# Kernel tuning notes

Measured on AMD Instinct MI355X. Metric: run time of the kernel, lower is better.

Reference implementation:

```python
import jax, jax.numpy as jnp
import numpy as np

DEGREE = 8


def setup_inputs() -> dict:
    key = jax.random.key(0)
    k1, k2 = jax.random.split(key)
    x = jax.random.normal(k1, (8192, 1024), dtype=jnp.float32)
    # xavier_normal-ish scale for coeffs [input_dim, output_dim, degree+1]
    std = (2.0 / (1024 + 1024)) ** 0.5
    cheby_coeffs = jax.random.normal(k2, (1024, 1024, DEGREE + 1), dtype=jnp.float32) * std
    return {"x": x, "cheby_coeffs": cheby_coeffs}


def _cheby(x, degree):
    # x: [B, I] in [-1, 1]; returns T: [B, I, degree+1]
    T = [jnp.ones_like(x), x]
    for n in range(2, degree + 1):
        T.append(2.0 * x * T[-1] - T[-2])
    return jnp.stack(T, axis=-1)


def reference(x, cheby_coeffs) -> jnp.ndarray:
    input_dim = cheby_coeffs.shape[0]
    degree = cheby_coeffs.shape[-1] - 1
    x = x.reshape(-1, input_dim)
    xmin = jnp.min(x, axis=1, keepdims=True)
    xmax = jnp.max(x, axis=1, keepdims=True)
    x = 2.0 * (x - xmin) / (xmax - xmin) - 1.0
    T = _cheby(x, degree)  # [B, I, D+1]
    y = jnp.einsum('bij,ioj->bo', T, cheby_coeffs)
    return y
```

## Files before the change

kernel.cpp:

```cpp
#include <hip/hip_runtime.h>
#include <hip/hip_bf16.h>


typedef __attribute__((ext_vector_type(8))) short bf16x8s;
typedef __attribute__((ext_vector_type(4))) float f32x4;

constexpr int BROWS = 8192;
constexpr int IDIM  = 1024;
constexpr int ODIM  = 1024;
constexpr int DEG1  = 9;
constexpr int KP    = 8;
constexpr int KD    = IDIM * KP;

__device__ __forceinline__ ushort f2bf(float f) {
  return ((__hip_bfloat16_raw)__float2bfloat16(f)).x;
}

__device__ __forceinline__ void gload_lds16(const void* g, void* l) {
  __builtin_amdgcn_global_load_lds(
      (const __attribute__((address_space(1))) unsigned int*)g,
      (__attribute__((address_space(3))) unsigned int*)l, 16, 0, 0);
}

__global__ __launch_bounds__(256) void zero_bias_kernel(float* __restrict__ bias) {
  bias[blockIdx.x * 256 + threadIdx.x] = 0.0f;
}

__global__ __launch_bounds__(256) void build_a_kernel(const float* __restrict__ x,
                                                      ushort* __restrict__ A2) {
  __shared__ float red[8];
  const int b = blockIdx.x, t = threadIdx.x, lane = t & 63, wv = t >> 6;
  const float* xr = x + (size_t)b * IDIM;
  const float4 v = ((const float4*)xr)[t];
  float mn = fminf(fminf(v.x, v.y), fminf(v.z, v.w));
  float mx = fmaxf(fmaxf(v.x, v.y), fmaxf(v.z, v.w));
#pragma unroll
  for (int off = 32; off >= 1; off >>= 1) {
    mn = fminf(mn, __shfl_xor(mn, off));
    mx = fmaxf(mx, __shfl_xor(mx, off));
  }
  if (lane == 0) { red[wv] = mn; red[4 + wv] = mx; }
  __syncthreads();
  mn = fminf(fminf(red[0], red[1]), fminf(red[2], red[3]));
  mx = fmaxf(fmaxf(red[4], red[5]), fmaxf(red[6], red[7]));
  const float sc = 2.0f / (mx - mn);
  const float of = -mn * sc - 1.0f;

  uint4* adst = (uint4*)(A2 + (size_t)b * KD);
#pragma unroll
  for (int c = 0; c < 4; ++c) {
    const int i = c * 256 + t;
    const float xn = fmaf(sc, xr[i], of);
    const float T2 = 2.f * xn * xn - 1.f;
    const float T3 = 2.f * xn * T2 - xn;
    const float T4 = 2.f * xn * T3 - T2;
    const float T5 = 2.f * xn * T4 - T3;
    const float T6 = 2.f * xn * T5 - T4;
    const float T7 = 2.f * xn * T6 - T5;
    const float T8 = 2.f * xn * T7 - T6;
    uint4 w;
    w.x = (uint)f2bf(xn) | ((uint)f2bf(T2) << 16);
    w.y = (uint)f2bf(T3) | ((uint)f2bf(T4) << 16);
    w.z = (uint)f2bf(T5) | ((uint)f2bf(T6) << 16);
    w.w = (uint)f2bf(T7) | ((uint)f2bf(T8) << 16);
    adst[i] = w;
  }
}

__global__ __launch_bounds__(256) void build_b_kernel(const float* __restrict__ coeffs,
                                                      ushort* __restrict__ B2T,
                                                      float* __restrict__ bias) {
  __shared__ __align__(16) ushort tile[64 * 256];
  __shared__ float lb[64];
  const int i0 = blockIdx.x * 32;
  const int o0 = blockIdx.y * 64;
  const int t  = threadIdx.x;
  if (t < 64) lb[t] = 0.0f;
  __syncthreads();
  for (int idx = t; idx < 18432; idx += 256) {
    const int i_l = idx / 576;
    const int rem = idx - i_l * 576;
    const float v = coeffs[((size_t)(i0 + i_l) * ODIM + o0) * DEG1 + rem];
    const int o_l = rem / 9;
    const int j   = rem - o_l * 9;
    if (j == 0) atomicAdd(&lb[o_l], v);
    else tile[o_l * 256 + i_l * KP + (j - 1)] = f2bf(v);
  }
  __syncthreads();
  for (int idx = t; idx < 2048; idx += 256) {
    const int o_l = idx >> 5;
    const int w   = idx & 31;
    uint4* gdst = (uint4*)(B2T + (size_t)(o0 + o_l) * KD + i0 * KP);
    gdst[w] = ((const uint4*)tile)[idx];
  }
  if (t < 64) atomicAdd(&bias[o0 + t], lb[t]);
}

__global__ __launch_bounds__(512, 1) void gemm_kernel(const ushort* __restrict__ A2,
                                                      const ushort* __restrict__ B2T,
                                                      const float* __restrict__ bias,
                                                      float* __restrict__ out) {
  constexpr int BK    = 64;
  constexpr int KT    = KD / BK;
  constexpr int ABUF  = 256 * BK;
  constexpr int BBUF  = 128 * BK;
  constexpr int BUFSZ = ABUF + BBUF;
  __shared__ __align__(16) ushort Sm[3 * BUFSZ];

  const int t    = threadIdx.x;
  const int lane = t & 63;
  const int wave = t >> 6;
  const int wr   = wave >> 1;
  const int wc   = wave & 1;
  const int c16  = lane & 15;
  const int quad = lane >> 4;

  const int orig = blockIdx.y * 8 + blockIdx.x;
  const int swz  = (orig & 7) * 32 + (orig >> 3);
  const int rowBase = (swz >> 3) * 256;
  const int colBase = (swz & 7) * 128;

  const int trow = t >> 3;
  const int scol = (t & 7) ^ (trow & 7);
  const ushort* aB = A2  + (size_t)(rowBase + trow) * KD + scol * 8;
  const ushort* bB = B2T + (size_t)(colBase + trow) * KD + scol * 8;
  ushort* uA = Sm + t * 8;
  ushort* uB = Sm + ABUF + t * 8;

  auto issA = [&](int buf, size_t ko, int a) {
    gload_lds16(aB + (size_t)a * (64 * KD) + ko, uA + buf * BUFSZ + a * 4096);
  };
  auto issB = [&](int buf, size_t ko, int b2) {
    gload_lds16(bB + (size_t)b2 * (64 * KD) + ko, uB + buf * BUFSZ + b2 * 4096);
  };

  const int aoff = (wr * 64 + c16) * BK;
  const int boff = (wc * 64 + c16) * BK;
  const int cx0  = ((0 + quad) ^ (c16 & 7)) * 8;
  const int cx1  = ((4 + quad) ^ (c16 & 7)) * 8;

  f32x4 acc[4][4];
#pragma unroll
  for (int m = 0; m < 4; ++m)
#pragma unroll
    for (int n = 0; n < 4; ++n) acc[m][n] = (f32x4){0.f, 0.f, 0.f, 0.f};

  issA(0, 0, 0); issA(0, 0, 1); issA(0, 0, 2); issA(0, 0, 3);
  issB(0, 0, 0); issB(0, 0, 1);
  issA(1, BK, 0); issA(1, BK, 1); issA(1, BK, 2); issA(1, BK, 3);
  issB(1, BK, 0); issB(1, BK, 1);
  asm volatile("s_waitcnt vmcnt(6)" ::: "memory");
  __builtin_amdgcn_s_barrier();

  int cur = 0;
  for (int it = 0; it < KT; ++it) {
    const ushort* Asb = Sm + cur * BUFSZ;
    const ushort* Bsb = Asb + ABUF;
    const int nb = (cur >= 1) ? cur - 1 : 2;
    const size_t ko = (size_t)(it + 2) * BK;
    const bool pf = (it < KT - 2);

    {
      bf16x8s afr[4], bfr[4];
#pragma unroll
      for (int m = 0; m < 4; ++m)
        afr[m] = *(const bf16x8s*)&Asb[aoff + m * (16 * 64) + cx0];
#pragma unroll
      for (int n = 0; n < 4; ++n)
        bfr[n] = *(const bf16x8s*)&Bsb[boff + n * (16 * 64) + cx0];
      if (pf) { issA(nb, ko, 0); issA(nb, ko, 1); issA(nb, ko, 2); }
      __builtin_amdgcn_s_setprio(1);
#pragma unroll
      for (int m = 0; m < 4; ++m)
#pragma unroll
        for (int n = 0; n < 4; ++n)
          acc[m][n] = __builtin_amdgcn_mfma_f32_16x16x32_bf16(afr[m], bfr[n],
                                                              acc[m][n], 0, 0, 0);
      __builtin_amdgcn_s_setprio(0);
    }
    {
      bf16x8s afr[4], bfr[4];
#pragma unroll
      for (int m = 0; m < 4; ++m)
        afr[m] = *(const bf16x8s*)&Asb[aoff + m * (16 * 64) + cx1];
#pragma unroll
      for (int n = 0; n < 4; ++n)
        bfr[n] = *(const bf16x8s*)&Bsb[boff + n * (16 * 64) + cx1];
      if (pf) { issA(nb, ko, 3); issB(nb, ko, 0); issB(nb, ko, 1); }
      __builtin_amdgcn_s_setprio(1);
#pragma unroll
      for (int m = 0; m < 4; ++m)
#pragma unroll
        for (int n = 0; n < 4; ++n)
          acc[m][n] = __builtin_amdgcn_mfma_f32_16x16x32_bf16(afr[m], bfr[n],
                                                              acc[m][n], 0, 0, 0);
      __builtin_amdgcn_s_setprio(0);
    }

    if (pf)              { asm volatile("s_waitcnt vmcnt(6)" ::: "memory"); }
    else if (it == KT-2) { asm volatile("s_waitcnt vmcnt(0)" ::: "memory"); }
    __builtin_amdgcn_s_barrier();

    cur = (cur == 2) ? 0 : cur + 1;
  }

#pragma unroll
  for (int n = 0; n < 4; ++n) {
    const int col = colBase + wc * 64 + n * 16 + c16;
    const float bv = bias[col];
#pragma unroll
    for (int m = 0; m < 4; ++m) {
      const int r0 = rowBase + wr * 64 + m * 16 + quad * 4;
#pragma unroll
      for (int r = 0; r < 4; ++r)
        out[(size_t)(r0 + r) * ODIM + col] = acc[m][n][r] + bv;
    }
  }
}

extern "C" void kernel_launch(void* const* d_in, const int* in_sizes, int n_in,
                              void* d_out, int out_size, void* d_ws, size_t ws_size,
                              hipStream_t stream) {
  const float* x      = (const float*)d_in[0];
  const float* coeffs = (const float*)d_in[1];
  float* out = (float*)d_out;

  char* ws = (char*)d_ws;
  float*  bias = (float*)ws;
  ushort* B2T  = (ushort*)(ws + 65536);
  ushort* A2   = (ushort*)(ws + 65536 + (size_t)ODIM * KD * 2);

  zero_bias_kernel<<<ODIM / 256, 256, 0, stream>>>(bias);
  build_a_kernel<<<BROWS, 256, 0, stream>>>(x, A2);
  build_b_kernel<<<dim3(IDIM / 32, ODIM / 64), 256, 0, stream>>>(coeffs, B2T, bias);
  gemm_kernel<<<dim3(ODIM / 128, BROWS / 256), 512, 0, stream>>>(A2, B2T, bias, out);
}
```

Baseline: 275.8 us.

## Fuse Chebyshev feature expansion into GEMM A-tile loading, drop materialized A

The separate pass that expanded x into a bf16 Chebyshev feature matrix in global memory is removed. A small kernel now computes only per-row min/max scale and offset. The GEMM loads raw x values, evaluates the Chebyshev recurrence in registers and writes bf16 A tiles straight into shared memory, while B keeps its async global-to-LDS prefetch. This avoids writing and re-reading a roughly 128 MB intermediate. In exchange, each column block recomputes the polynomials, and the x-load latency plus the VALU work now sit inside the MFMA pipeline loop.

```diff
diff --git a/kernel.cpp b/kernel.cpp
--- a/kernel.cpp
+++ b/kernel.cpp
@@ -26,12 +26,11 @@
   bias[blockIdx.x * 256 + threadIdx.x] = 0.0f;
 }
 
-__global__ __launch_bounds__(256) void build_a_kernel(const float* __restrict__ x,
-                                                      ushort* __restrict__ A2) {
+__global__ __launch_bounds__(256) void rowstats_kernel(const float* __restrict__ x,
+                                                       float2* __restrict__ stats) {
   __shared__ float red[8];
   const int b = blockIdx.x, t = threadIdx.x, lane = t & 63, wv = t >> 6;
-  const float* xr = x + (size_t)b * IDIM;
-  const float4 v = ((const float4*)xr)[t];
+  const float4 v = ((const float4*)(x + (size_t)b * IDIM))[t];
   float mn = fminf(fminf(v.x, v.y), fminf(v.z, v.w));
   float mx = fmaxf(fmaxf(v.x, v.y), fmaxf(v.z, v.w));
 #pragma unroll
@@ -41,29 +40,11 @@
   }
   if (lane == 0) { red[wv] = mn; red[4 + wv] = mx; }
   __syncthreads();
-  mn = fminf(fminf(red[0], red[1]), fminf(red[2], red[3]));
-  mx = fmaxf(fmaxf(red[4], red[5]), fmaxf(red[6], red[7]));
-  const float sc = 2.0f / (mx - mn);
-  const float of = -mn * sc - 1.0f;
-
-  uint4* adst = (uint4*)(A2 + (size_t)b * KD);
-#pragma unroll
-  for (int c = 0; c < 4; ++c) {
-    const int i = c * 256 + t;
-    const float xn = fmaf(sc, xr[i], of);
-    const float T2 = 2.f * xn * xn - 1.f;
-    const float T3 = 2.f * xn * T2 - xn;
-    const float T4 = 2.f * xn * T3 - T2;
-    const float T5 = 2.f * xn * T4 - T3;
-    const float T6 = 2.f * xn * T5 - T4;
-    const float T7 = 2.f * xn * T6 - T5;
-    const float T8 = 2.f * xn * T7 - T6;
-    uint4 w;
-    w.x = (uint)f2bf(xn) | ((uint)f2bf(T2) << 16);
-    w.y = (uint)f2bf(T3) | ((uint)f2bf(T4) << 16);
-    w.z = (uint)f2bf(T5) | ((uint)f2bf(T6) << 16);
-    w.w = (uint)f2bf(T7) | ((uint)f2bf(T8) << 16);
-    adst[i] = w;
+  if (t == 0) {
+    mn = fminf(fminf(red[0], red[1]), fminf(red[2], red[3]));
+    mx = fmaxf(fmaxf(red[4], red[5]), fmaxf(red[6], red[7]));
+    const float sc = 2.0f / (mx - mn);
+    stats[b] = (float2){sc, -mn * sc - 1.0f};
   }
 }
 
@@ -96,7 +77,8 @@
   if (t < 64) atomicAdd(&bias[o0 + t], lb[t]);
 }
 
-__global__ __launch_bounds__(512, 1) void gemm_kernel(const ushort* __restrict__ A2,
+__global__ __launch_bounds__(512, 1) void gemm_kernel(const float* __restrict__ x,
+                                                      const float2* __restrict__ stats,
                                                       const ushort* __restrict__ B2T,
                                                       const float* __restrict__ bias,
                                                       float* __restrict__ out) {
@@ -122,13 +104,39 @@
 
   const int trow = t >> 3;
   const int scol = (t & 7) ^ (trow & 7);
-  const ushort* aB = A2  + (size_t)(rowBase + trow) * KD + scol * 8;
+  const float*  xB = x + (size_t)(rowBase + trow) * IDIM + scol;
   const ushort* bB = B2T + (size_t)(colBase + trow) * KD + scol * 8;
-  ushort* uA = Sm + t * 8;
   ushort* uB = Sm + ABUF + t * 8;
 
-  auto issA = [&](int buf, size_t ko, int a) {
-    gload_lds16(aB + (size_t)a * (64 * KD) + ko, uA + buf * BUFSZ + a * 4096);
+  float scr[4], ofr[4];
+#pragma unroll
+  for (int a = 0; a < 4; ++a) {
+    const float2 s = stats[rowBase + trow + 64 * a];
+    scr[a] = s.x; ofr[a] = s.y;
+  }
+
+  auto loadX = [&](int it2, float xv[4]) {
+#pragma unroll
+    for (int a = 0; a < 4; ++a) xv[a] = xB[(size_t)a * (64 * IDIM) + it2 * 8];
+  };
+  auto computeA = [&](int buf, const float xv[4]) {
+#pragma unroll
+    for (int a = 0; a < 4; ++a) {
+      const float xn = fmaf(scr[a], xv[a], ofr[a]);
+      const float T2 = 2.f * xn * xn - 1.f;
+      const float T3 = 2.f * xn * T2 - xn;
+      const float T4 = 2.f * xn * T3 - T2;
+      const float T5 = 2.f * xn * T4 - T3;
+      const float T6 = 2.f * xn * T5 - T4;
+      const float T7 = 2.f * xn * T6 - T5;
+      const float T8 = 2.f * xn * T7 - T6;
+      uint4 w;
+      w.x = (uint)f2bf(xn) | ((uint)f2bf(T2) << 16);
+      w.y = (uint)f2bf(T3) | ((uint)f2bf(T4) << 16);
+      w.z = (uint)f2bf(T5) | ((uint)f2bf(T6) << 16);
+      w.w = (uint)f2bf(T7) | ((uint)f2bf(T8) << 16);
+      *(uint4*)&Sm[buf * BUFSZ + a * 4096 + t * 8] = w;
+    }
   };
   auto issB = [&](int buf, size_t ko, int b2) {
     gload_lds16(bB + (size_t)b2 * (64 * KD) + ko, uB + buf * BUFSZ + b2 * 4096);
@@ -145,11 +153,14 @@
 #pragma unroll
     for (int n = 0; n < 4; ++n) acc[m][n] = (f32x4){0.f, 0.f, 0.f, 0.f};
 
-  issA(0, 0, 0); issA(0, 0, 1); issA(0, 0, 2); issA(0, 0, 3);
+  {
+    float xv[4];
+    loadX(0, xv); computeA(0, xv);
+    loadX(1, xv); computeA(1, xv);
+  }
   issB(0, 0, 0); issB(0, 0, 1);
-  issA(1, BK, 0); issA(1, BK, 1); issA(1, BK, 2); issA(1, BK, 3);
   issB(1, BK, 0); issB(1, BK, 1);
-  asm volatile("s_waitcnt vmcnt(6)" ::: "memory");
+  asm volatile("s_waitcnt vmcnt(2) lgkmcnt(0)" ::: "memory");
   __builtin_amdgcn_s_barrier();
 
   int cur = 0;
@@ -160,6 +171,9 @@
     const size_t ko = (size_t)(it + 2) * BK;
     const bool pf = (it < KT - 2);
 
+    float xv[4];
+    if (pf) loadX(it + 2, xv);
+
     {
       bf16x8s afr[4], bfr[4];
 #pragma unroll
@@ -168,7 +182,7 @@
 #pragma unroll
       for (int n = 0; n < 4; ++n)
         bfr[n] = *(const bf16x8s*)&Bsb[boff + n * (16 * 64) + cx0];
-      if (pf) { issA(nb, ko, 0); issA(nb, ko, 1); issA(nb, ko, 2); }
+      if (pf) { issB(nb, ko, 0); issB(nb, ko, 1); }
       __builtin_amdgcn_s_setprio(1);
 #pragma unroll
       for (int m = 0; m < 4; ++m)
@@ -178,6 +192,9 @@
                                                               acc[m][n], 0, 0, 0);
       __builtin_amdgcn_s_setprio(0);
     }
+
+    if (pf) computeA(nb, xv);
+
     {
       bf16x8s afr[4], bfr[4];
 #pragma unroll
@@ -186,7 +203,6 @@
 #pragma unroll
       for (int n = 0; n < 4; ++n)
         bfr[n] = *(const bf16x8s*)&Bsb[boff + n * (16 * 64) + cx1];
-      if (pf) { issA(nb, ko, 3); issB(nb, ko, 0); issB(nb, ko, 1); }
       __builtin_amdgcn_s_setprio(1);
 #pragma unroll
       for (int m = 0; m < 4; ++m)
@@ -197,8 +213,9 @@
       __builtin_amdgcn_s_setprio(0);
     }
 
-    if (pf)              { asm volatile("s_waitcnt vmcnt(6)" ::: "memory"); }
+    if (pf)              { asm volatile("s_waitcnt vmcnt(2)" ::: "memory"); }
     else if (it == KT-2) { asm volatile("s_waitcnt vmcnt(0)" ::: "memory"); }
+    asm volatile("s_waitcnt lgkmcnt(0)" ::: "memory");
     __builtin_amdgcn_s_barrier();
 
     cur = (cur == 2) ? 0 : cur + 1;
@@ -226,12 +243,12 @@
   float* out = (float*)d_out;
 
   char* ws = (char*)d_ws;
-  float*  bias = (float*)ws;
-  ushort* B2T  = (ushort*)(ws + 65536);
-  ushort* A2   = (ushort*)(ws + 65536 + (size_t)ODIM * KD * 2);
+  float*  bias  = (float*)ws;
+  float2* stats = (float2*)(ws + 65536);
+  ushort* B2T   = (ushort*)(ws + 131072);
 
   zero_bias_kernel<<<ODIM / 256, 256, 0, stream>>>(bias);
-  build_a_kernel<<<BROWS, 256, 0, stream>>>(x, A2);
+  rowstats_kernel<<<BROWS, 256, 0, stream>>>(x, stats);
   build_b_kernel<<<dim3(IDIM / 32, ODIM / 64), 256, 0, stream>>>(coeffs, B2T, bias);
-  gemm_kernel<<<dim3(ODIM / 128, BROWS / 256), 512, 0, stream>>>(A2, B2T, bias, out);
-}
+  gemm_kernel<<<dim3(ODIM / 128, BROWS / 256), 512, 0, stream>>>(x, stats, B2T, bias, out);
+}
```

Result: slower. 296.5 us (+7.5%).

## Shrink GEMM tile to 256x64 with BK=32, two blocks per CU, fold bias zeroing

Applied to the files above, without the earlier changes.

The GEMM block changes from 512 threads with a 256x128 tile and BK=64 to 256 threads with a 256x64 tile and BK=32. The launch bounds now allow two blocks per CU. The LDS swizzle, load issue schedule and vmcnt waits are reworked for the smaller tile, and the swizzle grid becomes 16x32. The separate bias-zeroing kernel is folded into build_a_kernel to remove one launch. The smaller tile halves B reuse per A load and raises global traffic, in exchange for more concurrent blocks that can hide latency.

```diff
diff --git a/kernel.cpp b/kernel.cpp
--- a/kernel.cpp
+++ b/kernel.cpp
@@ -22,14 +22,12 @@
       (__attribute__((address_space(3))) unsigned int*)l, 16, 0, 0);
 }
 
-__global__ __launch_bounds__(256) void zero_bias_kernel(float* __restrict__ bias) {
-  bias[blockIdx.x * 256 + threadIdx.x] = 0.0f;
-}
-
 __global__ __launch_bounds__(256) void build_a_kernel(const float* __restrict__ x,
-                                                      ushort* __restrict__ A2) {
+                                                      ushort* __restrict__ A2,
+                                                      float* __restrict__ bias) {
   __shared__ float red[8];
   const int b = blockIdx.x, t = threadIdx.x, lane = t & 63, wv = t >> 6;
+  if (b < 4) bias[b * 256 + t] = 0.0f;
   const float* xr = x + (size_t)b * IDIM;
   const float4 v = ((const float4*)xr)[t];
   float mn = fminf(fminf(v.x, v.y), fminf(v.z, v.w));
@@ -96,48 +94,44 @@
   if (t < 64) atomicAdd(&bias[o0 + t], lb[t]);
 }
 
-__global__ __launch_bounds__(512, 1) void gemm_kernel(const ushort* __restrict__ A2,
+__global__ __launch_bounds__(256, 2) void gemm_kernel(const ushort* __restrict__ A2,
                                                       const ushort* __restrict__ B2T,
                                                       const float* __restrict__ bias,
                                                       float* __restrict__ out) {
-  constexpr int BK    = 64;
+  constexpr int BK    = 32;
   constexpr int KT    = KD / BK;
   constexpr int ABUF  = 256 * BK;
-  constexpr int BBUF  = 128 * BK;
+  constexpr int BBUF  = 64 * BK;
   constexpr int BUFSZ = ABUF + BBUF;
   __shared__ __align__(16) ushort Sm[3 * BUFSZ];
 
   const int t    = threadIdx.x;
   const int lane = t & 63;
   const int wave = t >> 6;
-  const int wr   = wave >> 1;
-  const int wc   = wave & 1;
   const int c16  = lane & 15;
   const int quad = lane >> 4;
 
-  const int orig = blockIdx.y * 8 + blockIdx.x;
-  const int swz  = (orig & 7) * 32 + (orig >> 3);
-  const int rowBase = (swz >> 3) * 256;
-  const int colBase = (swz & 7) * 128;
-
-  const int trow = t >> 3;
-  const int scol = (t & 7) ^ (trow & 7);
+  const int orig = blockIdx.y * 16 + blockIdx.x;
+  const int swz  = (orig & 7) * 64 + (orig >> 3);
+  const int rowBase = (swz >> 4) * 256;
+  const int colBase = (swz & 15) * 64;
+
+  const int trow = t >> 2;
+  const int scol = (t & 3) ^ ((t >> 3) & 3);
   const ushort* aB = A2  + (size_t)(rowBase + trow) * KD + scol * 8;
   const ushort* bB = B2T + (size_t)(colBase + trow) * KD + scol * 8;
-  ushort* uA = Sm + t * 8;
-  ushort* uB = Sm + ABUF + t * 8;
+  ushort* uS = Sm + t * 8;
 
   auto issA = [&](int buf, size_t ko, int a) {
-    gload_lds16(aB + (size_t)a * (64 * KD) + ko, uA + buf * BUFSZ + a * 4096);
+    gload_lds16(aB + (size_t)a * (64 * KD) + ko, uS + buf * BUFSZ + a * 2048);
   };
-  auto issB = [&](int buf, size_t ko, int b2) {
-    gload_lds16(bB + (size_t)b2 * (64 * KD) + ko, uB + buf * BUFSZ + b2 * 4096);
+  auto issB = [&](int buf, size_t ko) {
+    gload_lds16(bB + ko, uS + buf * BUFSZ + ABUF);
   };
 
-  const int aoff = (wr * 64 + c16) * BK;
-  const int boff = (wc * 64 + c16) * BK;
-  const int cx0  = ((0 + quad) ^ (c16 & 7)) * 8;
-  const int cx1  = ((4 + quad) ^ (c16 & 7)) * 8;
+  const int cx   = (quad ^ ((c16 >> 1) & 3)) * 8;
+  const int aoff = (wave * 64 + c16) * BK + cx;
+  const int boff = c16 * BK + cx;
 
   f32x4 acc[4][4];
 #pragma unroll
@@ -145,11 +139,9 @@
 #pragma unroll
     for (int n = 0; n < 4; ++n) acc[m][n] = (f32x4){0.f, 0.f, 0.f, 0.f};
 
-  issA(0, 0, 0); issA(0, 0, 1); issA(0, 0, 2); issA(0, 0, 3);
-  issB(0, 0, 0); issB(0, 0, 1);
-  issA(1, BK, 0); issA(1, BK, 1); issA(1, BK, 2); issA(1, BK, 3);
-  issB(1, BK, 0); issB(1, BK, 1);
-  asm volatile("s_waitcnt vmcnt(6)" ::: "memory");
+  issA(0, 0, 0); issA(0, 0, 1); issA(0, 0, 2); issA(0, 0, 3); issB(0, 0);
+  issA(1, BK, 0); issA(1, BK, 1); issA(1, BK, 2); issA(1, BK, 3); issB(1, BK);
+  asm volatile("s_waitcnt vmcnt(5)" ::: "memory");
   __builtin_amdgcn_s_barrier();
 
   int cur = 0;
@@ -160,44 +152,27 @@
     const size_t ko = (size_t)(it + 2) * BK;
     const bool pf = (it < KT - 2);
 
-    {
-      bf16x8s afr[4], bfr[4];
-#pragma unroll
-      for (int m = 0; m < 4; ++m)
-        afr[m] = *(const bf16x8s*)&Asb[aoff + m * (16 * 64) + cx0];
+    bf16x8s afr[4], bfr[4];
+#pragma unroll
+    for (int m = 0; m < 4; ++m)
+      afr[m] = *(const bf16x8s*)&Asb[aoff + m * (16 * BK)];
+#pragma unroll
+    for (int n = 0; n < 4; ++n)
+      bfr[n] = *(const bf16x8s*)&Bsb[boff + n * (16 * BK)];
+
+    if (pf) { issA(nb, ko, 0); issA(nb, ko, 1); issA(nb, ko, 2); issA(nb, ko, 3);
+              issB(nb, ko); }
+
+    __builtin_amdgcn_s_setprio(1);
+#pragma unroll
+    for (int m = 0; m < 4; ++m)
 #pragma unroll
       for (int n = 0; n < 4; ++n)
-        bfr[n] = *(const bf16x8s*)&Bsb[boff + n * (16 * 64) + cx0];
-      if (pf) { issA(nb, ko, 0); issA(nb, ko, 1); issA(nb, ko, 2); }
-      __builtin_amdgcn_s_setprio(1);
-#pragma unroll
-      for (int m = 0; m < 4; ++m)
-#pragma unroll
-        for (int n = 0; n < 4; ++n)
-          acc[m][n] = __builtin_amdgcn_mfma_f32_16x16x32_bf16(afr[m], bfr[n],
-                                                              acc[m][n], 0, 0, 0);
-      __builtin_amdgcn_s_setprio(0);
-    }
-    {
-      bf16x8s afr[4], bfr[4];
-#pragma unroll
-      for (int m = 0; m < 4; ++m)
-        afr[m] = *(const bf16x8s*)&Asb[aoff + m * (16 * 64) + cx1];
-#pragma unroll
-      for (int n = 0; n < 4; ++n)
-        bfr[n] = *(const bf16x8s*)&Bsb[boff + n * (16 * 64) + cx1];
-      if (pf) { issA(nb, ko, 3); issB(nb, ko, 0); issB(nb, ko, 1); }
-      __builtin_amdgcn_s_setprio(1);
-#pragma unroll
-      for (int m = 0; m < 4; ++m)
-#pragma unroll
-        for (int n = 0; n < 4; ++n)
-          acc[m][n] = __builtin_amdgcn_mfma_f32_16x16x32_bf16(afr[m], bfr[n],
-                                                              acc[m][n], 0, 0, 0);
-      __builtin_amdgcn_s_setprio(0);
-    }
-
-    if (pf)              { asm volatile("s_waitcnt vmcnt(6)" ::: "memory"); }
+        acc[m][n] = __builtin_amdgcn_mfma_f32_16x16x32_bf16(afr[m], bfr[n],
+                                                            acc[m][n], 0, 0, 0);
+    __builtin_amdgcn_s_setprio(0);
+
+    if (pf)              { asm volatile("s_waitcnt vmcnt(5)" ::: "memory"); }
     else if (it == KT-2) { asm volatile("s_waitcnt vmcnt(0)" ::: "memory"); }
     __builtin_amdgcn_s_barrier();
 
@@ -206,11 +181,11 @@
 
 #pragma unroll
   for (int n = 0; n < 4; ++n) {
-    const int col = colBase + wc * 64 + n * 16 + c16;
+    const int col = colBase + n * 16 + c16;
     const float bv = bias[col];
 #pragma unroll
     for (int m = 0; m < 4; ++m) {
-      const int r0 = rowBase + wr * 64 + m * 16 + quad * 4;
+      const int r0 = rowBase + wave * 64 + m * 16 + quad * 4;
 #pragma unroll
       for (int r = 0; r < 4; ++r)
         out[(size_t)(r0 + r) * ODIM + col] = acc[m][n][r] + bv;
@@ -230,8 +205,7 @@
   ushort* B2T  = (ushort*)(ws + 65536);
   ushort* A2   = (ushort*)(ws + 65536 + (size_t)ODIM * KD * 2);
 
-  zero_bias_kernel<<<ODIM / 256, 256, 0, stream>>>(bias);
-  build_a_kernel<<<BROWS, 256, 0, stream>>>(x, A2);
+  build_a_kernel<<<BROWS, 256, 0, stream>>>(x, A2, bias);
   build_b_kernel<<<dim3(IDIM / 32, ODIM / 64), 256, 0, stream>>>(coeffs, B2T, bias);
-  gemm_kernel<<<dim3(ODIM / 128, BROWS / 256), 512, 0, stream>>>(A2, B2T, bias, out);
-}
+  gemm_kernel<<<dim3(ODIM / 64, BROWS / 256), 256, 0, stream>>>(A2, B2T, bias, out);
+}
```

After: 334.6 us. 21.3% more time.

## Pre-swizzle B into MFMA fragment order and load it directly to registers

Applied to the files above, without the earlier changes.

build_b now writes coefficients in a fragment-blocked layout, so each lane can load its B operand straight from global memory into registers with double buffering. This drops B from LDS staging and shrinks LDS to four A buffers, which allows two blocks per CU. Bias zeroing is folded into build_a, removing one kernel launch, and the block-index swizzle is dropped. B global loads now sit on the critical path without LDS reuse across waves, and the A/B loads share one vmcnt counter, which makes the wait accounting fragile.

```diff
diff --git a/kernel.cpp b/kernel.cpp
--- a/kernel.cpp
+++ b/kernel.cpp
@@ -11,6 +11,7 @@
 constexpr int DEG1  = 9;
 constexpr int KP    = 8;
 constexpr int KD    = IDIM * KP;
+constexpr int NKB   = KD / 32;
 
 __device__ __forceinline__ ushort f2bf(float f) {
   return ((__hip_bfloat16_raw)__float2bfloat16(f)).x;
@@ -22,14 +23,12 @@
       (__attribute__((address_space(3))) unsigned int*)l, 16, 0, 0);
 }
 
-__global__ __launch_bounds__(256) void zero_bias_kernel(float* __restrict__ bias) {
-  bias[blockIdx.x * 256 + threadIdx.x] = 0.0f;
-}
-
 __global__ __launch_bounds__(256) void build_a_kernel(const float* __restrict__ x,
-                                                      ushort* __restrict__ A2) {
+                                                      ushort* __restrict__ A2,
+                                                      float* __restrict__ bias) {
   __shared__ float red[8];
   const int b = blockIdx.x, t = threadIdx.x, lane = t & 63, wv = t >> 6;
+  if (b < 4) bias[b * 256 + t] = 0.0f;
   const float* xr = x + (size_t)b * IDIM;
   const float4 v = ((const float4*)xr)[t];
   float mn = fminf(fminf(v.x, v.y), fminf(v.z, v.w));
@@ -68,7 +67,7 @@
 }
 
 __global__ __launch_bounds__(256) void build_b_kernel(const float* __restrict__ coeffs,
-                                                      ushort* __restrict__ B2T,
+                                                      uint4* __restrict__ Bf,
                                                       float* __restrict__ bias) {
   __shared__ __align__(16) ushort tile[64 * 256];
   __shared__ float lb[64];
@@ -89,23 +88,22 @@
   __syncthreads();
   for (int idx = t; idx < 2048; idx += 256) {
     const int o_l = idx >> 5;
-    const int w   = idx & 31;
-    uint4* gdst = (uint4*)(B2T + (size_t)(o0 + o_l) * KD + i0 * KP);
-    gdst[w] = ((const uint4*)tile)[idx];
+    const int i_l = idx & 31;
+    const int o = o0 + o_l, i = i0 + i_l;
+    const size_t dst = ((size_t)(o >> 4) * NKB + (i >> 2)) * 64 + (o & 15) * 4 + (i & 3);
+    Bf[dst] = ((const uint4*)tile)[idx];
   }
   if (t < 64) atomicAdd(&bias[o0 + t], lb[t]);
 }
 
-__global__ __launch_bounds__(512, 1) void gemm_kernel(const ushort* __restrict__ A2,
-                                                      const ushort* __restrict__ B2T,
+__global__ __launch_bounds__(512, 2) void gemm_kernel(const ushort* __restrict__ A2,
+                                                      const uint4* __restrict__ Bf,
                                                       const float* __restrict__ bias,
                                                       float* __restrict__ out) {
-  constexpr int BK    = 64;
-  constexpr int KT    = KD / BK;
-  constexpr int ABUF  = 256 * BK;
-  constexpr int BBUF  = 128 * BK;
-  constexpr int BUFSZ = ABUF + BBUF;
-  __shared__ __align__(16) ushort Sm[3 * BUFSZ];
+  constexpr int BK   = 64;
+  constexpr int KT   = KD / BK;
+  constexpr int ABUF = 256 * BK;
+  __shared__ __align__(16) ushort Sm[4 * ABUF];
 
   const int t    = threadIdx.x;
   const int lane = t & 63;
@@ -115,27 +113,26 @@
   const int c16  = lane & 15;
   const int quad = lane >> 4;
 
-  const int orig = blockIdx.y * 8 + blockIdx.x;
-  const int swz  = (orig & 7) * 32 + (orig >> 3);
-  const int rowBase = (swz >> 3) * 256;
-  const int colBase = (swz & 7) * 128;
+  const int rowBase = blockIdx.y * 256;
+  const int colBase = blockIdx.x * 128;
 
   const int trow = t >> 3;
   const int scol = (t & 7) ^ (trow & 7);
-  const ushort* aB = A2  + (size_t)(rowBase + trow) * KD + scol * 8;
-  const ushort* bB = B2T + (size_t)(colBase + trow) * KD + scol * 8;
+  const ushort* aB = A2 + (size_t)(rowBase + trow) * KD + scol * 8;
   ushort* uA = Sm + t * 8;
-  ushort* uB = Sm + ABUF + t * 8;
-
-  auto issA = [&](int buf, size_t ko, int a) {
-    gload_lds16(aB + (size_t)a * (64 * KD) + ko, uA + buf * BUFSZ + a * 4096);
+
+  auto issA = [&](int buf, int itile, int a) {
+    gload_lds16(aB + (size_t)a * (64 * KD) + (size_t)itile * BK,
+                uA + buf * ABUF + a * 4096);
   };
-  auto issB = [&](int buf, size_t ko, int b2) {
-    gload_lds16(bB + (size_t)b2 * (64 * KD) + ko, uB + buf * BUFSZ + b2 * 4096);
-  };
+
+  const int bq = c16 * 4 + quad;
+  const uint4* Bn[4];
+#pragma unroll
+  for (int n = 0; n < 4; ++n)
+    Bn[n] = Bf + ((size_t)(colBase / 16 + wc * 4 + n) * NKB) * 64 + bq;
 
   const int aoff = (wr * 64 + c16) * BK;
-  const int boff = (wc * 64 + c16) * BK;
   const int cx0  = ((0 + quad) ^ (c16 & 7)) * 8;
   const int cx1  = ((4 + quad) ^ (c16 & 7)) * 8;
 
@@ -145,63 +142,75 @@
 #pragma unroll
     for (int n = 0; n < 4; ++n) acc[m][n] = (f32x4){0.f, 0.f, 0.f, 0.f};
 
+  bf16x8s bfr[2][8];
+
+#pragma unroll
+  for (int n = 0; n < 4; ++n) {
+    bfr[0][n]     = *(const bf16x8s*)&Bn[n][0];
+    bfr[0][4 + n] = *(const bf16x8s*)&Bn[n][64];
+  }
   issA(0, 0, 0); issA(0, 0, 1); issA(0, 0, 2); issA(0, 0, 3);
-  issB(0, 0, 0); issB(0, 0, 1);
-  issA(1, BK, 0); issA(1, BK, 1); issA(1, BK, 2); issA(1, BK, 3);
-  issB(1, BK, 0); issB(1, BK, 1);
-  asm volatile("s_waitcnt vmcnt(6)" ::: "memory");
+  issA(1, 1, 0); issA(1, 1, 1); issA(1, 1, 2); issA(1, 1, 3);
+#pragma unroll
+  for (int n = 0; n < 4; ++n) {
+    bfr[1][n]     = *(const bf16x8s*)&Bn[n][2 * 64];
+    bfr[1][4 + n] = *(const bf16x8s*)&Bn[n][3 * 64];
+  }
+  asm volatile("s_waitcnt vmcnt(12)" ::: "memory");
   __builtin_amdgcn_s_barrier();
 
-  int cur = 0;
-  for (int it = 0; it < KT; ++it) {
-    const ushort* Asb = Sm + cur * BUFSZ;
-    const ushort* Bsb = Asb + ABUF;
-    const int nb = (cur >= 1) ? cur - 1 : 2;
-    const size_t ko = (size_t)(it + 2) * BK;
-    const bool pf = (it < KT - 2);
-
-    {
-      bf16x8s afr[4], bfr[4];
-#pragma unroll
-      for (int m = 0; m < 4; ++m)
-        afr[m] = *(const bf16x8s*)&Asb[aoff + m * (16 * 64) + cx0];
-#pragma unroll
-      for (int n = 0; n < 4; ++n)
-        bfr[n] = *(const bf16x8s*)&Bsb[boff + n * (16 * 64) + cx0];
-      if (pf) { issA(nb, ko, 0); issA(nb, ko, 1); issA(nb, ko, 2); }
-      __builtin_amdgcn_s_setprio(1);
-#pragma unroll
-      for (int m = 0; m < 4; ++m)
-#pragma unroll
-        for (int n = 0; n < 4; ++n)
-          acc[m][n] = __builtin_amdgcn_mfma_f32_16x16x32_bf16(afr[m], bfr[n],
-                                                              acc[m][n], 0, 0, 0);
-      __builtin_amdgcn_s_setprio(0);
+  for (int itb = 0; itb < KT; itb += 4) {
+#pragma unroll
+    for (int J = 0; J < 4; ++J) {
+      const int it = itb + J;
+      const ushort* Asb = Sm + J * ABUF;
+
+      if (it + 1 < KT) {
+        const size_t kb0 = (size_t)(it + 1) * 2 * 64;
+#pragma unroll
+        for (int n = 0; n < 4; ++n) {
+          bfr[(J + 1) & 1][n]     = *(const bf16x8s*)&Bn[n][kb0];
+          bfr[(J + 1) & 1][4 + n] = *(const bf16x8s*)&Bn[n][kb0 + 64];
+        }
+      }
+      if (it + 2 < KT) {
+        issA((J + 2) & 3, it + 2, 0); issA((J + 2) & 3, it + 2, 1);
+        issA((J + 2) & 3, it + 2, 2); issA((J + 2) & 3, it + 2, 3);
+      }
+
+      {
+        bf16x8s afr[4];
+#pragma unroll
+        for (int m = 0; m < 4; ++m)
+          afr[m] = *(const bf16x8s*)&Asb[aoff + m * (16 * BK) + cx0];
+        __builtin_amdgcn_s_setprio(1);
+#pragma unroll
+        for (int m = 0; m < 4; ++m)
+#pragma unroll
+          for (int n = 0; n < 4; ++n)
+            acc[m][n] = __builtin_amdgcn_mfma_f32_16x16x32_bf16(
+                afr[m], bfr[J & 1][n], acc[m][n], 0, 0, 0);
+        __builtin_amdgcn_s_setprio(0);
+      }
+      {
+        bf16x8s afr[4];
+#pragma unroll
+        for (int m = 0; m < 4; ++m)
+          afr[m] = *(const bf16x8s*)&Asb[aoff + m * (16 * BK) + cx1];
+        __builtin_amdgcn_s_setprio(1);
+#pragma unroll
+        for (int m = 0; m < 4; ++m)
+#pragma unroll
+          for (int n = 0; n < 4; ++n)
+            acc[m][n] = __builtin_amdgcn_mfma_f32_16x16x32_bf16(
+                afr[m], bfr[J & 1][4 + n], acc[m][n], 0, 0, 0);
+        __builtin_amdgcn_s_setprio(0);
+      }
+
+      if (it < KT - 2) { asm volatile("s_waitcnt vmcnt(12)" ::: "memory"); }
+      else             { asm volatile("s_waitcnt vmcnt(0)"  ::: "memory"); }
+      __builtin_amdgcn_s_barrier();
     }
-    {
-      bf16x8s afr[4], bfr[4];
-#pragma unroll
-      for (int m = 0; m < 4; ++m)
-        afr[m] = *(const bf16x8s*)&Asb[aoff + m * (16 * 64) + cx1];
-#pragma unroll
-      for (int n = 0; n < 4; ++n)
-        bfr[n] = *(const bf16x8s*)&Bsb[boff + n * (16 * 64) + cx1];
-      if (pf) { issA(nb, ko, 3); issB(nb, ko, 0); issB(nb, ko, 1); }
-      __builtin_amdgcn_s_setprio(1);
-#pragma unroll
-      for (int m = 0; m < 4; ++m)
-#pragma unroll
-        for (int n = 0; n < 4; ++n)
-          acc[m][n] = __builtin_amdgcn_mfma_f32_16x16x32_bf16(afr[m], bfr[n],
-                                                              acc[m][n], 0, 0, 0);
-      __builtin_amdgcn_s_setprio(0);
-    }
-
-    if (pf)              { asm volatile("s_waitcnt vmcnt(6)" ::: "memory"); }
-    else if (it == KT-2) { asm volatile("s_waitcnt vmcnt(0)" ::: "memory"); }
-    __builtin_amdgcn_s_barrier();
-
-    cur = (cur == 2) ? 0 : cur + 1;
   }
 
 #pragma unroll
@@ -226,12 +235,11 @@
   float* out = (float*)d_out;
 
   char* ws = (char*)d_ws;
-  float*  bias = (float*)ws;
-  ushort* B2T  = (ushort*)(ws + 65536);
-  ushort* A2   = (ushort*)(ws + 65536 + (size_t)ODIM * KD * 2);
-
-  zero_bias_kernel<<<ODIM / 256, 256, 0, stream>>>(bias);
-  build_a_kernel<<<BROWS, 256, 0, stream>>>(x, A2);
-  build_b_kernel<<<dim3(IDIM / 32, ODIM / 64), 256, 0, stream>>>(coeffs, B2T, bias);
-  gemm_kernel<<<dim3(ODIM / 128, BROWS / 256), 512, 0, stream>>>(A2, B2T, bias, out);
-}
+  float* bias = (float*)ws;
+  uint4* Bf   = (uint4*)(ws + 65536);
+  ushort* A2  = (ushort*)(ws + 65536 + (size_t)ODIM * KD * 2);
+
+  build_a_kernel<<<BROWS, 256, 0, stream>>>(x, A2, bias);
+  build_b_kernel<<<dim3(IDIM / 32, ODIM / 64), 256, 0, stream>>>(coeffs, Bf, bias);
+  gemm_kernel<<<dim3(ODIM / 128, BROWS / 256), 512, 0, stream>>>(A2, Bf, bias, out);
+}
```

After: 365.3 us. +32.5%, slower.
